# Kernel optimization log

Measured on AMD Instinct MI355X. Metric: run time of the kernel, lower is better.

Reference implementation:

```python
import jax, jax.numpy as jnp
import numpy as np

B, N, D, L = 16, 100, 1024, 2000


def setup_inputs() -> dict:
    key = jax.random.key(0)
    ks = jax.random.split(key, 9)
    s = 1.0 / np.sqrt(D)
    return {
        "feature": jax.random.normal(ks[0], (B, N, D), dtype=jnp.float32),
        "graph": jax.random.randint(ks[1], (B, N, N), 0, L),
        "W0": jax.random.normal(ks[2], (D, D), dtype=jnp.float32) * s,
        "W1": jax.random.normal(ks[3], (D, D), dtype=jnp.float32) * s,
        "bias": jax.random.uniform(ks[4], (L, D), dtype=jnp.float32, minval=-s, maxval=s),
        "dp_Wa": jax.random.normal(ks[5], (D, D), dtype=jnp.float32) * s,
        "dp_ba": jax.random.normal(ks[6], (D,), dtype=jnp.float32) * s,
        "dp_Wb": jax.random.normal(ks[7], (D, D), dtype=jnp.float32) * s,
        "dp_bb": jax.random.normal(ks[8], (D,), dtype=jnp.float32) * s,
        "get_alpha": 0,
    }


def reference(feature, graph, W0, W1, bias, dp_Wa, dp_ba, dp_Wb, dp_bb, get_alpha):
    # ---- DirectedGraphConv.conv ----
    adj = (graph != 0).astype(feature.dtype)                     # [B,N,N]
    out = feature + feature @ W0.T + feature @ W1.T              # [B,N,D]
    out = out + jnp.take(bias, graph, axis=0).sum(axis=2)        # label-embedding gather+sum over neighbors
    # ---- relation_alpha: DotProduct(feature, feature) ----
    a = feature @ dp_Wa.T + dp_ba                                # [B,N,D]
    b = feature @ dp_Wb.T + dp_bb                                # [B,N,D]
    alpha = jnp.einsum('bik,bjk->bij', a, b)                     # [B,N,N]
    alpha = jnp.maximum(alpha, 0.0)                              # alpha[alpha<0]=0
    alpha = jnp.einsum('bij,bjk->bik', adj, alpha)               # bmm(adj, alpha)
    alpha = jax.nn.softmax(alpha, axis=1)                        # Softmax(dim=1)
    out = jnp.einsum('bij,bjk->bik', alpha, out)                 # bmm(alpha, output)
    if get_alpha:
        return (out, alpha)
    return out
```

## Files before the change

### kernel.cpp

```cpp
#include <hip/hip_runtime.h>
#include <stdint.h>

#define B_   16
#define N_   100
#define D_   1024
#define L_   2000
#define M_   1600
#define KP   2048

#define RCAP 24
#define ZMAX 2400
#define TC   12

typedef __bf16 bf16x8 __attribute__((ext_vector_type(8)));
typedef float  f32x4  __attribute__((ext_vector_type(4)));

__device__ __forceinline__ void gl_lds16(const __bf16* g, __bf16* l) {
    __builtin_amdgcn_global_load_lds(
        (const __attribute__((address_space(1))) void*)g,
        (__attribute__((address_space(3))) void*)l, 16, 0, 0);
}


__global__ void __launch_bounds__(256)
k_prep(const float* __restrict__ f,
       const float* __restrict__ W0, const float* __restrict__ W1,
       const float* __restrict__ Wa, const float* __restrict__ Wb,
       const float* __restrict__ bias, const int* __restrict__ graph,
       __bf16* __restrict__ fb, __bf16* __restrict__ wcat,
       __bf16* __restrict__ biasBT, __bf16* __restrict__ cnt) {
    int bid = blockIdx.x, t = threadIdx.x;
    __shared__ float lds[32][33];
    __shared__ unsigned int hist[KP];

    if (bid < 2336) {
        int i = bid * 256 + t;
        union { __bf16 h[8]; uint4 u; } pk;
        if (i < 204800) {
            long base = (long)i * 8;
            const float4* p = (const float4*)(f + base);
            float4 x = p[0], y = p[1];
            pk.h[0]=(__bf16)x.x; pk.h[1]=(__bf16)x.y; pk.h[2]=(__bf16)x.z; pk.h[3]=(__bf16)x.w;
            pk.h[4]=(__bf16)y.x; pk.h[5]=(__bf16)y.y; pk.h[6]=(__bf16)y.z; pk.h[7]=(__bf16)y.w;
            ((uint4*)fb)[i] = pk.u;
        } else {
            int j = i - 204800;
            long base = (long)j * 8;
            long seg = base >> 20;
            long off = base & ((1l << 20) - 1);
            if (seg == 0) {
                const float4* p0 = (const float4*)(W0 + off);
                const float4* p1 = (const float4*)(W1 + off);
                float4 a0 = p0[0], a1 = p0[1], b0 = p1[0], b1 = p1[1];
                pk.h[0]=(__bf16)(a0.x+b0.x); pk.h[1]=(__bf16)(a0.y+b0.y);
                pk.h[2]=(__bf16)(a0.z+b0.z); pk.h[3]=(__bf16)(a0.w+b0.w);
                pk.h[4]=(__bf16)(a1.x+b1.x); pk.h[5]=(__bf16)(a1.y+b1.y);
                pk.h[6]=(__bf16)(a1.z+b1.z); pk.h[7]=(__bf16)(a1.w+b1.w);
            } else {
                const float* src = (seg == 1) ? Wa : Wb;
                const float4* p = (const float4*)(src + off);
                float4 x = p[0], y = p[1];
                pk.h[0]=(__bf16)x.x; pk.h[1]=(__bf16)x.y; pk.h[2]=(__bf16)x.z; pk.h[3]=(__bf16)x.w;
                pk.h[4]=(__bf16)y.x; pk.h[5]=(__bf16)y.y; pk.h[6]=(__bf16)y.z; pk.h[7]=(__bf16)y.w;
            }
            ((uint4*)wcat)[j] = pk.u;
        }
    } else if (bid < 4384) {
        int tb = bid - 2336;
        int lt = tb >> 5, dt = tb & 31;
        int l0 = lt * 32, d0 = dt * 32;
        int r = t >> 3, cq = (t & 7) * 4;
        float4 v = make_float4(0.f, 0.f, 0.f, 0.f);
        if (l0 + r < L_) v = *(const float4*)(bias + (long)(l0 + r) * D_ + d0 + cq);
        lds[r][cq]=v.x; lds[r][cq+1]=v.y; lds[r][cq+2]=v.z; lds[r][cq+3]=v.w;
        __syncthreads();
        union { __bf16 h[4]; uint2 u; } pk;
        #pragma unroll
        for (int q = 0; q < 4; ++q) pk.h[q] = (__bf16)lds[cq + q][r];
        *(uint2*)(biasBT + (long)(d0 + r) * KP + l0 + cq) = pk.u;
    } else {
        int m = bid - 4384;
        for (int k = t; k < KP; k += 256) hist[k] = 0u;
        __syncthreads();
        if (t < N_) atomicAdd(&hist[graph[(long)m * N_ + t]], 1u);
        __syncthreads();
        union { __bf16 h[8]; uint4 u; } pk;
        #pragma unroll
        for (int q = 0; q < 8; ++q) pk.h[q] = (__bf16)(float)hist[t * 8 + q];
        ((uint4*)(cnt + (long)m * KP))[t] = pk.u;
    }
}


#define BM 64
#define BN 128
#define BK 64

__global__ void __launch_bounds__(256)
k_gemmAll(const __bf16* __restrict__ fb, const __bf16* __restrict__ wcat,
          const __bf16* __restrict__ cnt, const __bf16* __restrict__ biasBT,
          const float* __restrict__ feat, const float* __restrict__ ba,
          const float* __restrict__ bbias,
          float* __restrict__ out0, float* __restrict__ aB, float* __restrict__ bB,
          float* __restrict__ out0add) {
    __shared__ __align__(16) __bf16 As[BM * BK];
    __shared__ __align__(16) __bf16 Bs[BN * BK];
    int t = threadIdx.x;
    int pid = blockIdx.x;
    int lane = t & 63, wave = t >> 6;
    int wr = wave & 1, wc = wave >> 1;
    int lrow = lane & 15, quad = lane >> 4;

    bool isBias = pid < 200;
    int bm, bn, lda, K;
    const __bf16 *Ag, *Bg;
    if (isBias) {
        int v = (pid & 7) * 25 + (pid >> 3);
        bm = v >> 3; bn = v & 7;
        Ag = cnt    + (long)(bm * BM) * KP;
        Bg = biasBT + (long)(bn * BN) * KP;
        lda = KP; K = KP;
    } else {
        int p2 = pid - 200;
        int v = (p2 & 7) * 75 + (p2 >> 3);
        bn = v / 25; bm = v % 25;
        Ag = fb   + (long)(bm * BM) * D_;
        Bg = wcat + (long)(bn * BN) * D_;
        lda = D_; K = D_;
    }

    f32x4 acc[2][4] = {};
    for (int k0 = 0; k0 < K; k0 += BK) {
        #pragma unroll
        for (int pi = 0; pi < 2; ++pi) {
            int p = pi * 256 + t, row = p >> 3, c = (p & 7) ^ (row & 7);
            gl_lds16(Ag + (long)row * lda + k0 + c * 8, As + p * 8);
        }
        #pragma unroll
        for (int pi = 0; pi < 4; ++pi) {
            int p = pi * 256 + t, row = p >> 3, c = (p & 7) ^ (row & 7);
            gl_lds16(Bg + (long)row * lda + k0 + c * 8, Bs + p * 8);
        }
        __syncthreads();
        #pragma unroll
        for (int ks = 0; ks < 2; ++ks) {
            bf16x8 af[2], bf[4];
            #pragma unroll
            for (int i = 0; i < 2; ++i) {
                int r = wr * 32 + i * 16 + lrow;
                int slot = r * 8 + (((ks << 2) | quad) ^ (r & 7));
                af[i] = *(const bf16x8*)(As + slot * 8);
            }
            #pragma unroll
            for (int j = 0; j < 4; ++j) {
                int r = wc * 64 + j * 16 + lrow;
                int slot = r * 8 + (((ks << 2) | quad) ^ (r & 7));
                bf[j] = *(const bf16x8*)(Bs + slot * 8);
            }
            #pragma unroll
            for (int i = 0; i < 2; ++i)
                #pragma unroll
                for (int j = 0; j < 4; ++j)
                    acc[i][j] = __builtin_amdgcn_mfma_f32_16x16x32_bf16(af[i], bf[j], acc[i][j], 0, 0, 0);
        }
        __syncthreads();
    }

    if (!isBias) {
        int nbase = bn * BN;
        int seg = bn >> 3;
        #pragma unroll
        for (int i = 0; i < 2; ++i) {
            int gm0 = bm * BM + wr * 32 + i * 16 + quad * 4;
            #pragma unroll
            for (int j = 0; j < 4; ++j) {
                int col = (nbase + wc * 64 + j * 16 + lrow) & 1023;
                #pragma unroll
                for (int r = 0; r < 4; ++r) {
                    long m = gm0 + r;
                    float v = acc[i][j][r];
                    if (seg == 0)      out0[m * D_ + col] = v + feat[m * D_ + col];
                    else if (seg == 1) aB[m * D_ + col]   = v + ba[col];
                    else               bB[m * D_ + col]   = v + bbias[col];
                }
            }
        }
    } else {
        #pragma unroll
        for (int i = 0; i < 2; ++i) {
            int gm0 = bm * BM + wr * 32 + i * 16 + quad * 4;
            #pragma unroll
            for (int j = 0; j < 4; ++j) {
                int col = bn * BN + wc * 64 + j * 16 + lrow;
                #pragma unroll
                for (int r = 0; r < 4; ++r) {
                    long m = gm0 + r;
                    out0add[m * D_ + col] = acc[i][j][r];
                }
            }
        }
    }
}


__global__ void __launch_bounds__(256)
k_alpha(const int* __restrict__ graph, const float* __restrict__ aB,
        const float* __restrict__ bB, float* __restrict__ wl, float* __restrict__ cwG) {
    __shared__ int rowCnt[N_], rowOff[N_], rowRank[N_];
    __shared__ int ndvS, totZS;
    __shared__ int zjL[ZMAX];
    __shared__ short prL[ZMAX];
    __shared__ float corrL[RCAP][4];
    __shared__ float wred[4][4];

    int pid = blockIdx.x;
    int b = pid / 25, kc = pid - b * 25;
    int t = threadIdx.x, lane = t & 63, wave = t >> 6;

    const int* g = graph + (long)b * N_ * N_;
    if (t < N_) {
        int c = 0;
        for (int j = 0; j < N_; ++j) if (g[t * N_ + j] == 0) ++c;
        rowCnt[t] = c;
    }
    if (t < RCAP * 4) corrL[t >> 2][t & 3] = 0.f;
    __syncthreads();
    if (t == 0) {
        int off = 0, rank = 0;
        for (int i = 0; i < N_; ++i) {
            if (rowCnt[i] > 0 && rank < RCAP) {
                rowRank[i] = rank; rowOff[i] = off; off += rowCnt[i]; ++rank;
            } else rowRank[i] = -1;
        }
        ndvS = rank; totZS = off;
    }
    __syncthreads();
    if (t < N_ && rowRank[t] >= 0) {
        int pos = rowOff[t], r = rowRank[t];
        for (int j = 0; j < N_; ++j)
            if (g[t * N_ + j] == 0) { zjL[pos] = j; prL[pos] = (short)r; ++pos; }
    }
    __syncthreads();
    int Z = totZS, ndv = ndvS;

    int k0 = kc * 4;
    float4 bv[4];
    #pragma unroll
    for (int kk = 0; kk < 4; ++kk)
        bv[kk] = *(const float4*)(bB + ((long)(b * N_ + k0 + kk)) * D_ + t * 4);

    for (int q = 0; q < Z; ++q) {
        const float* ar = aB + ((long)(b * N_ + zjL[q])) * D_;
        float4 av = *(const float4*)(ar + t * 4);
        float s[4];
        #pragma unroll
        for (int kk = 0; kk < 4; ++kk)
            s[kk] = av.x * bv[kk].x + av.y * bv[kk].y + av.z * bv[kk].z + av.w * bv[kk].w;
        #pragma unroll
        for (int off = 32; off > 0; off >>= 1)
            #pragma unroll
            for (int kk = 0; kk < 4; ++kk) s[kk] += __shfl_xor(s[kk], off);
        if (lane == 0) { wred[wave][0]=s[0]; wred[wave][1]=s[1]; wred[wave][2]=s[2]; wred[wave][3]=s[3]; }
        __syncthreads();
        if (t < 4) {
            float v = wred[0][t] + wred[1][t] + wred[2][t] + wred[3][t];
            corrL[prL[q]][t] += fmaxf(v, 0.f);
        }
        __syncthreads();
    }

    if (t < 4) {
        int k = k0 + t;
        float denom = (float)(N_ - ndv);
        for (int r = 0; r < ndv; ++r) {
            float e = __expf(-corrL[r][t]);
            corrL[r][t] = e;
            denom += e;
        }
        float w = 1.f / denom;
        wl[b * N_ + k] = w;
        for (int r = 0; r < ndv; ++r)
            cwG[((long)b * RCAP + r) * N_ + k] = corrL[r][t] * w;
    }
}


__global__ void __launch_bounds__(256)
k_mix(const int* __restrict__ graph, const float* __restrict__ wl,
      const float* __restrict__ cwG, const float* __restrict__ out0,
      const float* __restrict__ out0add, float* __restrict__ out) {
    int b = blockIdx.x, dq = blockIdx.y;
    int t = threadIdx.x, c4 = t & 63, q = t >> 6;
    int d0 = dq * 256;
    __shared__ int hasZ[N_], mapL[N_], ndvS;
    __shared__ float wT[TC][N_];
    __shared__ f32x4 parts[4][TC][64];

    const int* g = graph + (long)b * N_ * N_;
    if (t < N_) {
        int z = 0;
        for (int j = 0; j < N_; ++j) if (g[t * N_ + j] == 0) { z = 1; break; }
        hasZ[t] = z;
    }
    __syncthreads();
    if (t < N_) {
        int rank = 0;
        for (int i = 0; i < t; ++i) rank += hasZ[i];
        mapL[t] = (hasZ[t] && rank < RCAP) ? 1 + rank : 0;
    }
    if (t == 0) {
        int n = 0;
        for (int i = 0; i < N_; ++i) n += hasZ[i];
        ndvS = min(n, RCAP);
    }
    __syncthreads();
    int ndv = ndvS, ntask = ndv + 1;

    const float* o0 = out0    + (long)b * N_ * D_ + d0;
    const float* oa = out0add + (long)b * N_ * D_ + d0;
    for (int cb = 0; cb < ntask; cb += TC) {
        for (int idx = t; idx < TC * N_; idx += 256) {
            int rr = idx / N_, j = idx - rr * N_;
            int task = cb + rr;
            float v = 0.f;
            if (task == 0)         v = wl[b * N_ + j];
            else if (task <= ndv)  v = cwG[((long)b * RCAP + task - 1) * N_ + j];
            wT[rr][j] = v;
        }
        __syncthreads();
        f32x4 acc[TC] = {};
        for (int j = q * 25; j < q * 25 + 25; ++j) {
            f32x4 v = *(const f32x4*)(o0 + (long)j * D_ + c4 * 4)
                    + *(const f32x4*)(oa + (long)j * D_ + c4 * 4);
            #pragma unroll
            for (int rr = 0; rr < TC; ++rr) acc[rr] += wT[rr][j] * v;
        }
        #pragma unroll
        for (int rr = 0; rr < TC; ++rr) parts[q][rr][c4] = acc[rr];
        __syncthreads();
        for (int i = q * 25; i < q * 25 + 25; ++i) {
            int task = mapL[i];
            if (task >= cb && task < cb + TC) {
                int rr = task - cb;
                f32x4 s = parts[0][rr][c4] + parts[1][rr][c4]
                        + parts[2][rr][c4] + parts[3][rr][c4];
                *(f32x4*)(out + ((long)(b * N_ + i)) * D_ + d0 + c4 * 4) = s;
            }
        }
        __syncthreads();
    }
}


extern "C" void kernel_launch(void* const* d_in, const int* in_sizes, int n_in,
                              void* d_out, int out_size, void* d_ws, size_t ws_size,
                              hipStream_t stream) {
    const float* feature = (const float*)d_in[0];
    const int*   graph   = (const int*)d_in[1];
    const float* W0      = (const float*)d_in[2];
    const float* W1      = (const float*)d_in[3];
    const float* bias    = (const float*)d_in[4];
    const float* dp_Wa   = (const float*)d_in[5];
    const float* dp_ba   = (const float*)d_in[6];
    const float* dp_Wb   = (const float*)d_in[7];
    const float* dp_bb   = (const float*)d_in[8];
    float* out = (float*)d_out;

    char* w = (char*)d_ws;
    __bf16* fb16    = (__bf16*)(w);
    __bf16* wcat    = (__bf16*)(w + 3276800);
    __bf16* cnt     = (__bf16*)(w + 9568256);
    __bf16* biasBT  = (__bf16*)(w + 16121856);
    float*  out0    = (float*)(w + 20316160);
    float*  aB      = (float*)(w + 26869760);
    float*  bB      = (float*)(w + 33423360);
    float*  wl      = (float*)(w + 39976960);
    float*  cwG     = (float*)(w + 39983360);
    float*  out0add = (float*)(w + 40136960);

    k_prep<<<5984, 256, 0, stream>>>(feature, W0, W1, dp_Wa, dp_Wb, bias, graph,
                                     fb16, wcat, biasBT, cnt);
    k_gemmAll<<<800, 256, 0, stream>>>(fb16, wcat, cnt, biasBT, feature, dp_ba, dp_bb,
                                       out0, aB, bB, out0add);
    k_alpha<<<400, 256, 0, stream>>>(graph, aB, bB, wl, cwG);
    k_mix<<<dim3(B_, 4), 256, 0, stream>>>(graph, wl, cwG, out0, out0add, out);
}
```

Measured before the change: 173.0 us.

## Fuse W0+W1 and bias-count GEMMs via K-concatenated operands

Lays out feature and neighbor-label counts side by side as one A matrix (K=3072), with the combined W0+W1 weights and the transposed bias table side by side as the matching B matrix. One GEMM now produces out0 directly, so the separate out0add buffer, its store and its reload in the mix kernel go away, and the grid shrinks from 800 to 600 blocks. The alpha and mix kernels now read the label-0 histogram count instead of rescanning the graph for zero entries. The trade-off is longer K loops in the merged blocks, which may hurt tail balance across CUs.

```diff
diff --git a/kernel.cpp b/kernel.cpp
--- a/kernel.cpp
+++ b/kernel.cpp
@@ -7,6 +7,7 @@
 #define L_   2000
 #define M_   1600
 #define KP   2048
+#define AK   3072
 
 #define RCAP 24
 #define ZMAX 2400
@@ -27,8 +28,8 @@
        const float* __restrict__ W0, const float* __restrict__ W1,
        const float* __restrict__ Wa, const float* __restrict__ Wb,
        const float* __restrict__ bias, const int* __restrict__ graph,
-       __bf16* __restrict__ fb, __bf16* __restrict__ wcat,
-       __bf16* __restrict__ biasBT, __bf16* __restrict__ cnt) {
+       __bf16* __restrict__ Acat, __bf16* __restrict__ B0cat,
+       __bf16* __restrict__ wcat12) {
     int bid = blockIdx.x, t = threadIdx.x;
     __shared__ float lds[32][33];
     __shared__ unsigned int hist[KP];
@@ -42,13 +43,15 @@
             float4 x = p[0], y = p[1];
             pk.h[0]=(__bf16)x.x; pk.h[1]=(__bf16)x.y; pk.h[2]=(__bf16)x.z; pk.h[3]=(__bf16)x.w;
             pk.h[4]=(__bf16)y.x; pk.h[5]=(__bf16)y.y; pk.h[6]=(__bf16)y.z; pk.h[7]=(__bf16)y.w;
-            ((uint4*)fb)[i] = pk.u;
+            int m = i >> 7, c = i & 127;
+            ((uint4*)Acat)[(long)m * 384 + c] = pk.u;
         } else {
             int j = i - 204800;
             long base = (long)j * 8;
             long seg = base >> 20;
-            long off = base & ((1l << 20) - 1);
+            int  js  = j & 131071;
             if (seg == 0) {
+                long off = (long)js * 8;
                 const float4* p0 = (const float4*)(W0 + off);
                 const float4* p1 = (const float4*)(W1 + off);
                 float4 a0 = p0[0], a1 = p0[1], b0 = p1[0], b1 = p1[1];
@@ -56,14 +59,17 @@
                 pk.h[2]=(__bf16)(a0.z+b0.z); pk.h[3]=(__bf16)(a0.w+b0.w);
                 pk.h[4]=(__bf16)(a1.x+b1.x); pk.h[5]=(__bf16)(a1.y+b1.y);
                 pk.h[6]=(__bf16)(a1.z+b1.z); pk.h[7]=(__bf16)(a1.w+b1.w);
+                int row = js >> 7, c = js & 127;
+                ((uint4*)B0cat)[(long)row * 384 + c] = pk.u;
             } else {
                 const float* src = (seg == 1) ? Wa : Wb;
+                long off = (long)js * 8;
                 const float4* p = (const float4*)(src + off);
                 float4 x = p[0], y = p[1];
                 pk.h[0]=(__bf16)x.x; pk.h[1]=(__bf16)x.y; pk.h[2]=(__bf16)x.z; pk.h[3]=(__bf16)x.w;
                 pk.h[4]=(__bf16)y.x; pk.h[5]=(__bf16)y.y; pk.h[6]=(__bf16)y.z; pk.h[7]=(__bf16)y.w;
-            }
-            ((uint4*)wcat)[j] = pk.u;
+                ((uint4*)wcat12)[(long)(seg - 1) * 131072 + js] = pk.u;
+            }
         }
     } else if (bid < 4384) {
         int tb = bid - 2336;
@@ -77,7 +83,7 @@
         union { __bf16 h[4]; uint2 u; } pk;
         #pragma unroll
         for (int q = 0; q < 4; ++q) pk.h[q] = (__bf16)lds[cq + q][r];
-        *(uint2*)(biasBT + (long)(d0 + r) * KP + l0 + cq) = pk.u;
+        *(uint2*)(B0cat + (long)(d0 + r) * AK + 1024 + l0 + cq) = pk.u;
     } else {
         int m = bid - 4384;
         for (int k = t; k < KP; k += 256) hist[k] = 0u;
@@ -87,7 +93,7 @@
         union { __bf16 h[8]; uint4 u; } pk;
         #pragma unroll
         for (int q = 0; q < 8; ++q) pk.h[q] = (__bf16)(float)hist[t * 8 + q];
-        ((uint4*)(cnt + (long)m * KP))[t] = pk.u;
+        ((uint4*)(Acat + (long)m * AK + 1024))[t] = pk.u;
     }
 }
 
@@ -97,12 +103,11 @@
 #define BK 64
 
 __global__ void __launch_bounds__(256)
-k_gemmAll(const __bf16* __restrict__ fb, const __bf16* __restrict__ wcat,
-          const __bf16* __restrict__ cnt, const __bf16* __restrict__ biasBT,
+k_gemmAll(const __bf16* __restrict__ Acat, const __bf16* __restrict__ B0cat,
+          const __bf16* __restrict__ wcat12,
           const float* __restrict__ feat, const float* __restrict__ ba,
           const float* __restrict__ bbias,
-          float* __restrict__ out0, float* __restrict__ aB, float* __restrict__ bB,
-          float* __restrict__ out0add) {
+          float* __restrict__ out0, float* __restrict__ aB, float* __restrict__ bB) {
     __shared__ __align__(16) __bf16 As[BM * BK];
     __shared__ __align__(16) __bf16 Bs[BN * BK];
     int t = threadIdx.x;
@@ -111,22 +116,23 @@
     int wr = wave & 1, wc = wave >> 1;
     int lrow = lane & 15, quad = lane >> 4;
 
-    bool isBias = pid < 200;
-    int bm, bn, lda, K;
+    bool isMerged = pid < 200;
+    int bm, bn, K;
+    long ldb;
     const __bf16 *Ag, *Bg;
-    if (isBias) {
+    if (isMerged) {
         int v = (pid & 7) * 25 + (pid >> 3);
         bm = v >> 3; bn = v & 7;
-        Ag = cnt    + (long)(bm * BM) * KP;
-        Bg = biasBT + (long)(bn * BN) * KP;
-        lda = KP; K = KP;
+        Ag = Acat  + (long)(bm * BM) * AK;
+        Bg = B0cat + (long)(bn * BN) * AK;
+        ldb = AK; K = AK;
     } else {
         int p2 = pid - 200;
-        int v = (p2 & 7) * 75 + (p2 >> 3);
-        bn = v / 25; bm = v % 25;
-        Ag = fb   + (long)(bm * BM) * D_;
-        Bg = wcat + (long)(bn * BN) * D_;
-        lda = D_; K = D_;
+        int v = (p2 & 7) * 50 + (p2 >> 3);
+        bn = v / 25; bm = v - bn * 25;
+        Ag = Acat   + (long)(bm * BM) * AK;
+        Bg = wcat12 + (long)(bn * BN) * 1024;
+        ldb = 1024; K = 1024;
     }
 
     f32x4 acc[2][4] = {};
@@ -134,12 +140,12 @@
         #pragma unroll
         for (int pi = 0; pi < 2; ++pi) {
             int p = pi * 256 + t, row = p >> 3, c = (p & 7) ^ (row & 7);
-            gl_lds16(Ag + (long)row * lda + k0 + c * 8, As + p * 8);
+            gl_lds16(Ag + (long)row * AK + k0 + c * 8, As + p * 8);
         }
         #pragma unroll
         for (int pi = 0; pi < 4; ++pi) {
             int p = pi * 256 + t, row = p >> 3, c = (p & 7) ^ (row & 7);
-            gl_lds16(Bg + (long)row * lda + k0 + c * 8, Bs + p * 8);
+            gl_lds16(Bg + (long)row * ldb + k0 + c * 8, Bs + p * 8);
         }
         __syncthreads();
         #pragma unroll
@@ -166,7 +172,21 @@
         __syncthreads();
     }
 
-    if (!isBias) {
+    if (isMerged) {
+        #pragma unroll
+        for (int i = 0; i < 2; ++i) {
+            int gm0 = bm * BM + wr * 32 + i * 16 + quad * 4;
+            #pragma unroll
+            for (int j = 0; j < 4; ++j) {
+                int col = bn * BN + wc * 64 + j * 16 + lrow;
+                #pragma unroll
+                for (int r = 0; r < 4; ++r) {
+                    long m = gm0 + r;
+                    out0[m * D_ + col] = acc[i][j][r] + feat[m * D_ + col];
+                }
+            }
+        }
+    } else {
         int nbase = bn * BN;
         int seg = bn >> 3;
         #pragma unroll
@@ -179,33 +199,19 @@
                 for (int r = 0; r < 4; ++r) {
                     long m = gm0 + r;
                     float v = acc[i][j][r];
-                    if (seg == 0)      out0[m * D_ + col] = v + feat[m * D_ + col];
-                    else if (seg == 1) aB[m * D_ + col]   = v + ba[col];
-                    else               bB[m * D_ + col]   = v + bbias[col];
+                    if (seg == 0) aB[m * D_ + col] = v + ba[col];
+                    else          bB[m * D_ + col] = v + bbias[col];
                 }
             }
         }
-    } else {
-        #pragma unroll
-        for (int i = 0; i < 2; ++i) {
-            int gm0 = bm * BM + wr * 32 + i * 16 + quad * 4;
-            #pragma unroll
-            for (int j = 0; j < 4; ++j) {
-                int col = bn * BN + wc * 64 + j * 16 + lrow;
-                #pragma unroll
-                for (int r = 0; r < 4; ++r) {
-                    long m = gm0 + r;
-                    out0add[m * D_ + col] = acc[i][j][r];
-                }
-            }
-        }
     }
 }
 
 
 __global__ void __launch_bounds__(256)
-k_alpha(const int* __restrict__ graph, const float* __restrict__ aB,
-        const float* __restrict__ bB, float* __restrict__ wl, float* __restrict__ cwG) {
+k_alpha(const int* __restrict__ graph, const __bf16* __restrict__ Acat,
+        const float* __restrict__ aB, const float* __restrict__ bB,
+        float* __restrict__ wl, float* __restrict__ cwG) {
     __shared__ int rowCnt[N_], rowOff[N_], rowRank[N_];
     __shared__ int ndvS, totZS;
     __shared__ int zjL[ZMAX];
@@ -218,11 +224,8 @@
     int t = threadIdx.x, lane = t & 63, wave = t >> 6;
 
     const int* g = graph + (long)b * N_ * N_;
-    if (t < N_) {
-        int c = 0;
-        for (int j = 0; j < N_; ++j) if (g[t * N_ + j] == 0) ++c;
-        rowCnt[t] = c;
-    }
+    if (t < N_)
+        rowCnt[t] = (int)(float)Acat[(long)(b * N_ + t) * AK + 1024];
     if (t < RCAP * 4) corrL[t >> 2][t & 3] = 0.f;
     __syncthreads();
     if (t == 0) {
@@ -286,9 +289,9 @@
 
 
 __global__ void __launch_bounds__(256)
-k_mix(const int* __restrict__ graph, const float* __restrict__ wl,
+k_mix(const __bf16* __restrict__ Acat, const float* __restrict__ wl,
       const float* __restrict__ cwG, const float* __restrict__ out0,
-      const float* __restrict__ out0add, float* __restrict__ out) {
+      float* __restrict__ out) {
     int b = blockIdx.x, dq = blockIdx.y;
     int t = threadIdx.x, c4 = t & 63, q = t >> 6;
     int d0 = dq * 256;
@@ -296,12 +299,8 @@
     __shared__ float wT[TC][N_];
     __shared__ f32x4 parts[4][TC][64];
 
-    const int* g = graph + (long)b * N_ * N_;
-    if (t < N_) {
-        int z = 0;
-        for (int j = 0; j < N_; ++j) if (g[t * N_ + j] == 0) { z = 1; break; }
-        hasZ[t] = z;
-    }
+    if (t < N_)
+        hasZ[t] = ((float)Acat[(long)(b * N_ + t) * AK + 1024] > 0.f) ? 1 : 0;
     __syncthreads();
     if (t < N_) {
         int rank = 0;
@@ -316,8 +315,7 @@
     __syncthreads();
     int ndv = ndvS, ntask = ndv + 1;
 
-    const float* o0 = out0    + (long)b * N_ * D_ + d0;
-    const float* oa = out0add + (long)b * N_ * D_ + d0;
+    const float* o0 = out0 + (long)b * N_ * D_ + d0;
     for (int cb = 0; cb < ntask; cb += TC) {
         for (int idx = t; idx < TC * N_; idx += 256) {
             int rr = idx / N_, j = idx - rr * N_;
@@ -330,8 +328,7 @@
         __syncthreads();
         f32x4 acc[TC] = {};
         for (int j = q * 25; j < q * 25 + 25; ++j) {
-            f32x4 v = *(const f32x4*)(o0 + (long)j * D_ + c4 * 4)
-                    + *(const f32x4*)(oa + (long)j * D_ + c4 * 4);
+            f32x4 v = *(const f32x4*)(o0 + (long)j * D_ + c4 * 4);
             #pragma unroll
             for (int rr = 0; rr < TC; ++rr) acc[rr] += wT[rr][j] * v;
         }
@@ -367,21 +364,19 @@
     float* out = (float*)d_out;
 
     char* w = (char*)d_ws;
-    __bf16* fb16    = (__bf16*)(w);
-    __bf16* wcat    = (__bf16*)(w + 3276800);
-    __bf16* cnt     = (__bf16*)(w + 9568256);
-    __bf16* biasBT  = (__bf16*)(w + 16121856);
-    float*  out0    = (float*)(w + 20316160);
-    float*  aB      = (float*)(w + 26869760);
-    float*  bB      = (float*)(w + 33423360);
-    float*  wl      = (float*)(w + 39976960);
-    float*  cwG     = (float*)(w + 39983360);
-    float*  out0add = (float*)(w + 40136960);
+    __bf16* Acat   = (__bf16*)(w);
+    __bf16* B0cat  = (__bf16*)(w + 9830400);
+    __bf16* wcat12 = (__bf16*)(w + 16121856);
+    float*  out0   = (float*)(w + 20316160);
+    float*  aB     = (float*)(w + 26869760);
+    float*  bB     = (float*)(w + 33423360);
+    float*  wl     = (float*)(w + 39976960);
+    float*  cwG    = (float*)(w + 39983360);
 
     k_prep<<<5984, 256, 0, stream>>>(feature, W0, W1, dp_Wa, dp_Wb, bias, graph,
-                                     fb16, wcat, biasBT, cnt);
-    k_gemmAll<<<800, 256, 0, stream>>>(fb16, wcat, cnt, biasBT, feature, dp_ba, dp_bb,
-                                       out0, aB, bB, out0add);
-    k_alpha<<<400, 256, 0, stream>>>(graph, aB, bB, wl, cwG);
-    k_mix<<<dim3(B_, 4), 256, 0, stream>>>(graph, wl, cwG, out0, out0add, out);
-}
+                                     Acat, B0cat, wcat12);
+    k_gemmAll<<<600, 256, 0, stream>>>(Acat, B0cat, wcat12, feature, dp_ba, dp_bb,
+                                       out0, aB, bB);
+    k_alpha<<<400, 256, 0, stream>>>(graph, Acat, aB, bB, wl, cwG);
+    k_mix<<<dim3(B_, 4), 256, 0, stream>>>(Acat, wl, cwG, out0, out);
+}
```

Measured after the change: 173.4 us. About the same (+0.2%).
